# Performance work log

Measured on AMD Instinct MI355X. Metric: run time of the kernel, lower is better.

## Reference

```python
import jax, jax.numpy as jnp
import numpy as np
from jax import lax

EPS = 1e-5

def _conv(x, w, b, stride, pad):
    y = lax.conv_general_dilated(x, w, (stride, stride), ((pad, pad), (pad, pad)),
                                 dimension_numbers=('NCHW', 'OIHW', 'NCHW'))
    return y + b[None, :, None, None]

def _deconv(x, w, b):
    # torch ConvTranspose2d(k=4, s=2, p=1): weight (Cin, Cout, 4, 4)
    w2 = jnp.flip(w, (2, 3)).transpose(1, 0, 2, 3)  # OIHW for forward conv
    y = lax.conv_general_dilated(x, w2, (1, 1), ((2, 2), (2, 2)),
                                 lhs_dilation=(2, 2),
                                 dimension_numbers=('NCHW', 'OIHW', 'NCHW'))
    return y + b[None, :, None, None]

def _bn(x, g, b):
    m = jnp.mean(x, axis=(0, 2, 3), keepdims=True)
    v = jnp.mean((x - m) ** 2, axis=(0, 2, 3), keepdims=True)
    return g[None, :, None, None] * (x - m) * lax.rsqrt(v + EPS) + b[None, :, None, None]

def setup_inputs() -> dict:
    key = jax.random.key(0)
    ks = jax.random.split(key, 16)
    f32 = jnp.float32
    def w(k, shape):
        return (jax.random.normal(k, shape, f32) * 0.05)
    inp = {
        'x': jax.random.uniform(ks[0], (32, 1, 512, 512), f32),
        'w1': w(ks[1], (16, 1, 4, 4)),  'b1': jnp.zeros((16,), f32), 'g1': jnp.ones((16,), f32), 'be1': jnp.zeros((16,), f32),
        'w2': w(ks[2], (16, 16, 4, 4)), 'b2': jnp.zeros((16,), f32), 'g2': jnp.ones((16,), f32), 'be2': jnp.zeros((16,), f32),
        'w3': w(ks[3], (4, 16, 4, 4)),  'b3': jnp.zeros((4,), f32),  'g3': jnp.ones((4,), f32),  'be3': jnp.zeros((4,), f32),
        'wpre': w(ks[4], (2, 4, 1, 1)), 'bpre': jnp.zeros((2,), f32),
        'codebook': w(ks[5], (256, 2)),
        'wpost': w(ks[6], (4, 2, 1, 1)), 'bpost': jnp.zeros((4,), f32),
        'wd1': w(ks[7], (4, 16, 4, 4)),  'bd1': jnp.zeros((16,), f32), 'g4': jnp.ones((16,), f32), 'be4': jnp.zeros((16,), f32),
        'wd2': w(ks[8], (16, 16, 4, 4)), 'bd2': jnp.zeros((16,), f32), 'g5': jnp.ones((16,), f32), 'be5': jnp.zeros((16,), f32),
        'wd3': w(ks[9], (16, 1, 4, 4)),  'bd3': jnp.zeros((1,), f32),
    }
    return inp

def _forward(x, w1, b1, g1, be1, w2, b2, g2, be2, w3, b3, g3, be3,
             wpre, bpre, codebook, wpost, bpost,
             wd1, bd1, g4, be4, wd2, bd2, g5, be5, wd3, bd3):
    # encoder: three stride-2 convs with BN + ReLU
    h = jax.nn.relu(_bn(_conv(x, w1, b1, 2, 1), g1, be1))
    h = jax.nn.relu(_bn(_conv(h, w2, b2, 2, 1), g2, be2))
    h = jax.nn.relu(_bn(_conv(h, w3, b3, 2, 1), g3, be3))
    q = _conv(h, wpre, bpre, 1, 0)          # [B, 2, H/8, W/8]
    B, C, Hq, Wq = q.shape
    qf = q.transpose(0, 2, 3, 1).reshape(B * Hq * Wq, C)   # [N, 2]
    # squared Euclidean distances to codebook (argmin equals cdist argmin)
    d2 = (jnp.sum(qf * qf, -1, keepdims=True)
          - 2.0 * qf @ codebook.T
          + jnp.sum(codebook * codebook, -1)[None, :])     # [N, 256]
    idx = jnp.argmin(d2, axis=-1)
    quant = codebook[idx]                                   # gather [N, 2]
    commitment_loss = jnp.mean((lax.stop_gradient(quant) - qf) ** 2)
    codebook_loss = jnp.mean((quant - lax.stop_gradient(qf)) ** 2)
    qout = qf + lax.stop_gradient(quant - qf)               # straight-through
    qout = qout.reshape(B, Hq, Wq, C).transpose(0, 3, 1, 2)
    d = _conv(qout, wpost, bpost, 1, 0)
    d = jax.nn.relu(_bn(_deconv(d, wd1, bd1), g4, be4))
    d = jax.nn.relu(_bn(_deconv(d, wd2, bd2), g5, be5))
    out = jax.nn.sigmoid(_deconv(d, wd3, bd3))
    recon = jnp.mean((x - out) ** 2)
    total = 1.0 * recon + codebook_loss + 0.2 * commitment_loss
    return out, total

def reference(x, w1, b1, g1, be1, w2, b2, g2, be2, w3, b3, g3, be3,
              wpre, bpre, codebook, wpost, bpost,
              wd1, bd1, g4, be4, wd2, bd2, g5, be5, wd3, bd3):
    return _forward(x, w1, b1, g1, be1, w2, b2, g2, be2, w3, b3, g3, be3,
                    wpre, bpre, codebook, wpost, bpost,
                    wd1, bd1, g4, be4, wd2, bd2, g5, be5, wd3, bd3)
```

## Files before the change

kernel.cpp:

```cpp
#include <hip/hip_runtime.h>
#include <hip/hip_bf16.h>
#include <math.h>

using bf16 = __hip_bfloat16;

__device__ __forceinline__ float b2f(bf16 v) { return __bfloat162float(v); }
__device__ __forceinline__ float ldv(const void* p, size_t i, int m) {
  return m ? b2f(((const bf16*)p)[i]) : ((const float*)p)[i];
}

struct D2 { double s, s2; };

__device__ __forceinline__ void block_stats1(float v, D2* slot) {
  float v2 = v * v;
#pragma unroll
  for (int o = 32; o; o >>= 1) { v += __shfl_down(v, o, 64); v2 += __shfl_down(v2, o, 64); }
  __shared__ float a1[4], a2[4];
  int lane = threadIdx.x & 63, w = threadIdx.x >> 6;
  if (lane == 0) { a1[w] = v; a2[w] = v2; }
  __syncthreads();
  if (threadIdx.x == 0) {
    slot->s  = (double)a1[0] + a1[1] + a1[2] + a1[3];
    slot->s2 = (double)a2[0] + a2[1] + a2[2] + a2[3];
  }
}

__device__ __forceinline__ void block_stats1d4(const double* v, const double* vq, D2* base, int NB, int bx) {
  __shared__ double q1[16], q2[16];
  int lane = threadIdx.x & 63, w = threadIdx.x >> 6;
#pragma unroll
  for (int k = 0; k < 4; k++) {
    double s = v[k], s2 = vq[k];
#pragma unroll
    for (int o = 32; o; o >>= 1) { s += __shfl_down(s, o, 64); s2 += __shfl_down(s2, o, 64); }
    if (lane == 0) { q1[k * 4 + w] = s; q2[k * 4 + w] = s2; }
  }
  __syncthreads();
  if (threadIdx.x < 4) {
    int k = threadIdx.x;
    base[k * NB + bx].s  = q1[k * 4] + q1[k * 4 + 1] + q1[k * 4 + 2] + q1[k * 4 + 3];
    base[k * NB + bx].s2 = q2[k * 4] + q2[k * 4 + 1] + q2[k * 4 + 2] + q2[k * 4 + 3];
  }
}

__device__ __forceinline__ void block_sum1(float v, double* slot) {
#pragma unroll
  for (int o = 32; o; o >>= 1) v += __shfl_down(v, o, 64);
  __shared__ float a1[4];
  int lane = threadIdx.x & 63, w = threadIdx.x >> 6;
  if (lane == 0) a1[w] = v;
  __syncthreads();
  if (threadIdx.x == 0) *slot = (double)a1[0] + a1[1] + a1[2] + a1[3];
}

__device__ __forceinline__ void block_stats16(const float* vs, const float* vq, D2* base, int NB, int bx) {
  __shared__ float s1[64], s2[64];
  int lane = threadIdx.x & 63, w = threadIdx.x >> 6;
#pragma unroll
  for (int co = 0; co < 16; co++) {
    float v = vs[co], v2 = vq[co];
#pragma unroll
    for (int o = 32; o; o >>= 1) { v += __shfl_down(v, o, 64); v2 += __shfl_down(v2, o, 64); }
    if (lane == 0) { s1[co * 4 + w] = v; s2[co * 4 + w] = v2; }
  }
  __syncthreads();
  if (threadIdx.x < 16) {
    int co = threadIdx.x;
    base[co * NB + bx].s  = (double)s1[co * 4] + s1[co * 4 + 1] + s1[co * 4 + 2] + s1[co * 4 + 3];
    base[co * NB + bx].s2 = (double)s2[co * 4] + s2[co * 4 + 1] + s2[co * 4 + 2] + s2[co * 4 + 3];
  }
}

__global__ void init_k(const unsigned* __restrict__ xw, int* flag) {
  unsigned lo = xw[threadIdx.x] & 0xFFFFu;
  int inr = (lo >= 0x3000u && lo < 0x4000u) ? 1 : 0;
  unsigned long long b = __ballot(inr);
  __shared__ int cnt[4];
  if ((threadIdx.x & 63) == 0) cnt[threadIdx.x >> 6] = __popcll(b);
  __syncthreads();
  if (threadIdx.x == 0) *flag = (cnt[0] + cnt[1] + cnt[2] + cnt[3] >= 128) ? 1 : 0;
}

__global__ void prep_k(const void* w1, const void* b1, const void* w2, const void* b2,
                       const void* w3, const void* b3, const void* wpre, const void* bpre,
                       const void* cbk, const void* wpost, const void* bpost,
                       const void* wd1, const void* bd1, const void* wd2, const void* bd2,
                       const void* wd3, const void* bd3,
                       const void* g1, const void* be1, const void* g2, const void* be2,
                       const void* g3, const void* be3, const void* g4, const void* be4,
                       const void* g5, const void* be5,
                       float* __restrict__ PF, double* __restrict__ PD, const int* modep) {
  int m = *modep, t = threadIdx.x;
  for (int i = t; i < 256; i += 256) PF[i] = ldv(w1, i, m);
  if (t < 16) PF[256 + t] = ldv(b1, t, m);
  for (int i = t; i < 4096; i += 256) {
    int cig = i >> 10, tap = (i >> 6) & 15, c4 = (i >> 4) & 3, co = i & 15;
    PF[272 + i] = ldv(w2, co * 256 + (cig * 4 + c4) * 16 + tap, m);
  }
  if (t < 16) PF[4368 + t] = ldv(b2, t, m);
  for (int i = t; i < 1024; i += 256) {
    int co = i >> 6, ci = (i >> 4) & 3, tap = i & 15;
    PF[4384 + i] = ldv(wd1, ci * 256 + co * 16 + tap, m);
  }
  for (int i = t; i < 1024; i += 256) {
    int ci = i >> 8, tap = (i >> 4) & 15, co = i & 15;
    PF[14368 + i] = ldv(wd1, ci * 256 + co * 16 + tap, m);
  }
  if (t < 16) PF[5408 + t] = ldv(bd1, t, m);
  for (int i = t; i < 4096; i += 256) {
    int co = i >> 8, ci = (i >> 4) & 15, tap = i & 15;
    PF[5424 + i] = ldv(wd2, ci * 256 + co * 16 + tap, m);
  }
  for (int i = t; i < 4096; i += 256) {
    int ci = i >> 8, tap = (i >> 4) & 15, co = i & 15;
    PF[10272 + i] = ldv(wd2, ci * 256 + co * 16 + tap, m);
  }
  if (t < 16) PF[9520 + t] = ldv(bd2, t, m);
  for (int i = t; i < 256; i += 256) PF[9536 + i] = ldv(wd3, i, m);
  {
    int tap = t >> 4, ci = t & 15;
    PF[10016 + t] = ldv(wd3, ci * 16 + tap, m);
  }
  if (t == 0) PF[9792] = ldv(bd3, 0, m);
  if (t < 16) {
    PF[9856 + t] = ldv(g1, t, m);  PF[9872 + t] = ldv(be1, t, m);
    PF[9888 + t] = ldv(g2, t, m);  PF[9904 + t] = ldv(be2, t, m);
    PF[9952 + t] = ldv(g4, t, m);  PF[9968 + t] = ldv(be4, t, m);
    PF[9984 + t] = ldv(g5, t, m);  PF[10000 + t] = ldv(be5, t, m);
  }
  if (t < 4) { PF[9920 + t] = ldv(g3, t, m); PF[9936 + t] = ldv(be3, t, m); }
  for (int i = t; i < 1024; i += 256) PD[i] = ldv(w3, i, m);
  if (t < 4) PD[1024 + t] = ldv(b3, t, m);
  if (t < 8) PD[1028 + t] = ldv(wpre, t, m);
  if (t < 2) PD[1036 + t] = ldv(bpre, t, m);
  for (int i = t; i < 512; i += 256) PD[1040 + i] = ldv(cbk, i, m);
  if (t < 8) PD[1552 + t] = ldv(wpost, t, m);
  if (t < 4) PD[1560 + t] = ldv(bpost, t, m);
}

__global__ __launch_bounds__(256) void bn_reduce_k(const D2* __restrict__ part, int NB,
                                                   double* __restrict__ stD, float* __restrict__ stF,
                                                   const float* __restrict__ gb, double invN) {
  int c = blockIdx.x;
  double s = 0, s2 = 0;
  for (int i = threadIdx.x; i < NB; i += 256) { D2 p = part[c * NB + i]; s += p.s; s2 += p.s2; }
#pragma unroll
  for (int o = 32; o; o >>= 1) { s += __shfl_down(s, o, 64); s2 += __shfl_down(s2, o, 64); }
  __shared__ double l1[4], l2[4];
  int lane = threadIdx.x & 63, w = threadIdx.x >> 6;
  if (lane == 0) { l1[w] = s; l2[w] = s2; }
  __syncthreads();
  if (threadIdx.x == 0) {
    double S = l1[0] + l1[1] + l1[2] + l1[3], Q = l2[0] + l2[1] + l2[2] + l2[3];
    double mu = S * invN, var = Q * invN - mu * mu;
    if (var < 0) var = 0;
    double sc = (double)gb[c] / sqrt(var + 1e-5);
    double sh = (double)gb[16 + c] - mu * sc;
    stD[c] = sc; stD[16 + c] = sh;
    stF[c] = (float)sc; stF[16 + c] = (float)sh;
  }
}

__global__ __launch_bounds__(256) void conv1_t(const void* __restrict__ x, const float* __restrict__ PF,
                                               float* __restrict__ y, D2* __restrict__ part,
                                               const int* modep) {
  const int m = *modep;
  __shared__ float sx[10 * 130];
  int t = threadIdx.x;
  int bx = blockIdx.x;
  int b = bx >> 8, r = bx & 255, tY = r >> 2, tX = r & 3;
  int iy0 = 8 * tY - 1, ix0 = 128 * tX - 1;
  size_t xb = (size_t)b * 262144;
  for (int i = t; i < 1300; i += 256) {
    int ry = i / 130, rx = i - ry * 130;
    int gy = iy0 + ry, gx = ix0 + rx;
    float v = 0.f;
    if ((unsigned)gy < 512u && (unsigned)gx < 512u) v = ldv(x, xb + (size_t)gy * 512 + gx, m);
    sx[i] = v;
  }
  __syncthreads();
  int tyy = t >> 6, txx = t & 63;
  int oy = tY * 4 + tyy, ox = tX * 64 + txx;
  float acc[16];
#pragma unroll
  for (int co = 0; co < 16; co++) acc[co] = PF[256 + co];
  int ly = 2 * tyy, lx = 2 * txx;
#pragma unroll
  for (int ky = 0; ky < 4; ky++) {
#pragma unroll
    for (int kx = 0; kx < 4; kx++) {
      float v = sx[(ly + ky) * 130 + lx + kx];
#pragma unroll
      for (int co = 0; co < 16; co++) acc[co] = fmaf(v, PF[co * 16 + ky * 4 + kx], acc[co]);
    }
  }
  size_t pix = (size_t)b * 65536 + (size_t)(oy * 256 + ox);
  *(float4*)(y + 0 * 8388608 + pix * 4) = make_float4(acc[0],  acc[1],  acc[2],  acc[3]);
  *(float4*)(y + 1 * 8388608 + pix * 4) = make_float4(acc[4],  acc[5],  acc[6],  acc[7]);
  *(float4*)(y + 2 * 8388608 + pix * 4) = make_float4(acc[8],  acc[9],  acc[10], acc[11]);
  *(float4*)(y + 3 * 8388608 + pix * 4) = make_float4(acc[12], acc[13], acc[14], acc[15]);
  float vq_[16];
#pragma unroll
  for (int co = 0; co < 16; co++) vq_[co] = acc[co] * acc[co];
  block_stats16(acc, vq_, part, 8192, bx);
}

__device__ __forceinline__ float4 aff_relu4(float4 v, float4 sc, float4 sh) {
  v.x = fmaxf(fmaf(v.x, sc.x, sh.x), 0.f);
  v.y = fmaxf(fmaf(v.y, sc.y, sh.y), 0.f);
  v.z = fmaxf(fmaf(v.z, sc.z, sh.z), 0.f);
  v.w = fmaxf(fmaf(v.w, sc.w, sh.w), 0.f);
  return v;
}

__global__ __launch_bounds__(256, 8) void conv2_t(const float* __restrict__ h1, const float* __restrict__ PF,
                                                  const float* __restrict__ aff, float* __restrict__ h2,
                                                  D2* __restrict__ part) {
  __shared__ float su[4896];
  int t = threadIdx.x, ty = t >> 4, tx = t & 15;
  int bx = blockIdx.x, bb = bx >> 6, r = bx & 63, tY = r >> 3, tX = r & 7;
  int oy = tY * 16 + ty, ox = tX * 16 + tx;
  int iy0 = 32 * tY - 1, ix0 = 32 * tX - 1;
  const float* W2 = PF + 272;
  const float4* A4 = (const float4*)aff;
  float acc[16];
#pragma unroll
  for (int co = 0; co < 16; co++) acc[co] = PF[4368 + co];
#pragma unroll
  for (int g = 0; g < 4; g++) {
    __syncthreads();
    float4 SC = A4[g], SH = A4[4 + g];
    const float* pg = h1 + (size_t)g * 8388608 + (size_t)bb * 262144;
    for (int i = t; i < 1156; i += 256) {
      int riy = i / 34, rix = i - riy * 34;
      int gy = iy0 + riy, gx = ix0 + rix;
      float4 v = make_float4(0.f, 0.f, 0.f, 0.f);
      if ((unsigned)gy < 256u && (unsigned)gx < 256u)
        v = aff_relu4(*(const float4*)(pg + (size_t)(gy * 256 + gx) * 4), SC, SH);
      int s = (rix & 1) * 2448 + riy * 18 + (rix >> 1);
      su[s] = v.x; su[612 + s] = v.y; su[1224 + s] = v.z; su[1836 + s] = v.w;
    }
    __syncthreads();
    const float* wg = W2 + g * 1024;
    int base = 2 * ty * 18 + tx;
#pragma unroll
    for (int ky = 0; ky < 4; ky++) {
#pragma unroll
      for (int kx = 0; kx < 4; kx++) {
        int s = (kx & 1) * 2448 + ky * 18 + (kx >> 1) + base;
        float v0 = su[s], v1 = su[612 + s], v2 = su[1224 + s], v3 = su[1836 + s];
        const float* wt = wg + (ky * 4 + kx) * 64;
#pragma unroll
        for (int co = 0; co < 16; co++) {
          float s0 = fmaf(v0, wt[co], acc[co]);
          float s1 = fmaf(v1, wt[16 + co], s0);
          float s2 = fmaf(v2, wt[32 + co], s1);
          acc[co] = fmaf(v3, wt[48 + co], s2);
        }
      }
    }
  }
  float vq_[16];
#pragma unroll
  for (int co = 0; co < 16; co++) {
    h2[((size_t)(bb * 16 + co) * 128 + oy) * 128 + ox] = acc[co];
    vq_[co] = acc[co] * acc[co];
  }
  block_stats16(acc, vq_, part, 2048, bx);
}

__global__ __launch_bounds__(256) void conv3_k(const float* __restrict__ h2, const double* __restrict__ PD,
                                               const float* __restrict__ aff, double* __restrict__ c3,
                                               D2* __restrict__ part) {
  int idx = blockIdx.x * 256 + threadIdx.x;
  int b = idx >> 12, rem = idx & 4095, oy = rem >> 6, ox = rem & 63;
  double a0 = PD[1024], a1 = PD[1025], a2 = PD[1026], a3 = PD[1027];
  int iy0 = 2 * oy - 1, ix0 = 2 * ox - 1;
  for (int ci = 0; ci < 16; ci++) {
    const float* ib = h2 + (size_t)(b * 16 + ci) * 16384;
    float sc = aff[ci], sh = aff[16 + ci];
    const double* wr = PD + ci * 16;
#pragma unroll
    for (int ky = 0; ky < 4; ky++) {
      int iy = iy0 + ky;
      if ((unsigned)iy < 128u) {
        const float* row = ib + iy * 128;
#pragma unroll
        for (int kx = 0; kx < 4; kx++) {
          int ix = ix0 + kx;
          if ((unsigned)ix < 128u) {
            double v = (double)fmaxf(fmaf(row[ix], sc, sh), 0.f);
            int tp = ky * 4 + kx;
            a0 = fma(v, wr[tp], a0);
            a1 = fma(v, wr[256 + tp], a1);
            a2 = fma(v, wr[512 + tp], a2);
            a3 = fma(v, wr[768 + tp], a3);
          }
        }
      }
    }
  }
  size_t cb = (size_t)b * 16384 + rem;
  c3[cb] = a0; c3[cb + 4096] = a1; c3[cb + 8192] = a2; c3[cb + 12288] = a3;
  double vs[4] = {a0, a1, a2, a3};
  double vq[4] = {a0 * a0, a1 * a1, a2 * a2, a3 * a3};
  block_stats1d4(vs, vq, part, 512, blockIdx.x);
}

__global__ __launch_bounds__(256) void vq_k(const double* __restrict__ c3, const double* __restrict__ PD,
                                            const double* __restrict__ stD2, float* __restrict__ d0,
                                            double* __restrict__ vp) {
  __shared__ double cb[512];
  for (int i = threadIdx.x; i < 512; i += 256) cb[i] = PD[1040 + i];
  __syncthreads();
  int pix = blockIdx.x * 256 + threadIdx.x;
  int b = pix >> 12, rem = pix & 4095;
  const double* hb = c3 + (size_t)b * 16384 + rem;
  double q0 = PD[1036], q1 = PD[1037];
#pragma unroll
  for (int ci = 0; ci < 4; ci++) {
    double v = fma(hb[ci * 4096], stD2[ci], stD2[16 + ci]);
    if (v < 0) v = 0;
    q0 = fma(v, PD[1028 + ci], q0);
    q1 = fma(v, PD[1032 + ci], q1);
  }
  int best = 0;
  double bd = 1e300;
  for (int k = 0; k < 256; k++) {
    double dx = q0 - cb[2 * k], dy = q1 - cb[2 * k + 1];
    double d = dx * dx + dy * dy;
    if (d < bd) { bd = d; best = k; }
  }
  double c0 = cb[2 * best], c1 = cb[2 * best + 1];
  double e0 = q0 - c0, e1 = q1 - c1;
  float* ob = d0 + (size_t)b * 16384 + rem;
#pragma unroll
  for (int c = 0; c < 4; c++)
    ob[c * 4096] = (float)(PD[1560 + c] + PD[1552 + 2 * c] * c0 + PD[1552 + 2 * c + 1] * c1);
  double v = e0 * e0 + e1 * e1;
#pragma unroll
  for (int o = 32; o; o >>= 1) v += __shfl_down(v, o, 64);
  __shared__ double l1[4];
  int lane = threadIdx.x & 63, w = threadIdx.x >> 6;
  if (lane == 0) l1[w] = v;
  __syncthreads();
  if (threadIdx.x == 0) vp[blockIdx.x] = l1[0] + l1[1] + l1[2] + l1[3];
}

__global__ __launch_bounds__(256) void deconv1_k(const float* __restrict__ d0, const float* __restrict__ PF,
                                                 float* __restrict__ d1, D2* __restrict__ part) {
  int phase = blockIdx.y, a = phase >> 1, bc = phase & 1;
  int idx = blockIdx.x * 256 + threadIdx.x;
  int b = idx >> 12, rem = idx & 4095, qy = rem >> 6, qx = rem & 63;
  const float* WT = PF + 14368;
  float acc[16];
#pragma unroll
  for (int co = 0; co < 16; co++) acc[co] = PF[5408 + co];
  const float* hb = d0 + (size_t)b * 16384;
#pragma unroll
  for (int t2y = 0; t2y < 2; t2y++) {
    int iy = qy + a - t2y;
    if ((unsigned)iy < 64u) {
      int kyo = (1 - a + 2 * t2y) * 4;
#pragma unroll
      for (int t2x = 0; t2x < 2; t2x++) {
        int ix = qx + bc - t2x;
        if ((unsigned)ix < 64u) {
          int tap = kyo + (1 - bc + 2 * t2x);
          int off = iy * 64 + ix;
#pragma unroll
          for (int ci = 0; ci < 4; ci++) {
            float v = hb[ci * 4096 + off];
            const float* wt = WT + ci * 256 + tap * 16;
#pragma unroll
            for (int co = 0; co < 16; co++) acc[co] = fmaf(v, wt[co], acc[co]);
          }
        }
      }
    }
  }
  int oy = 2 * qy + a, ox = 2 * qx + bc;
  size_t pix = (size_t)b * 16384 + (size_t)(oy * 128 + ox);
  *(float4*)(d1 + 0 * 2097152 + pix * 4) = make_float4(acc[0],  acc[1],  acc[2],  acc[3]);
  *(float4*)(d1 + 1 * 2097152 + pix * 4) = make_float4(acc[4],  acc[5],  acc[6],  acc[7]);
  *(float4*)(d1 + 2 * 2097152 + pix * 4) = make_float4(acc[8],  acc[9],  acc[10], acc[11]);
  *(float4*)(d1 + 3 * 2097152 + pix * 4) = make_float4(acc[12], acc[13], acc[14], acc[15]);
  float vq_[16];
#pragma unroll
  for (int co = 0; co < 16; co++) vq_[co] = acc[co] * acc[co];
  block_stats16(acc, vq_, part, 2048, blockIdx.y * 512 + blockIdx.x);
}

__global__ __launch_bounds__(256) void deconv2_t(const float* __restrict__ d1, const float* __restrict__ PF,
                                                 const float* __restrict__ aff, float* __restrict__ d2,
                                                 D2* __restrict__ part) {
  __shared__ float su[16 * 324];
  int t = threadIdx.x, py = t >> 4, px = t & 15;
  int bx = blockIdx.x, bb = bx >> 6, r = bx & 63, tY = r >> 3, tX = r & 7;
  int iy0 = 16 * tY - 1, ix0 = 16 * tX - 1;
  const float4* A4 = (const float4*)aff;
  for (int i = t; i < 1296; i += 256) {
    int g = i / 324, rr = i - g * 324;
    int riy = rr / 18, rix = rr - riy * 18;
    int gy = iy0 + riy, gx = ix0 + rix;
    float4 v = make_float4(0.f, 0.f, 0.f, 0.f);
    if ((unsigned)gy < 128u && (unsigned)gx < 128u)
      v = aff_relu4(*(const float4*)(d1 + (size_t)g * 2097152 +
                                     ((size_t)bb * 16384 + (size_t)(gy * 128 + gx)) * 4),
                    A4[g], A4[4 + g]);
    int s0 = g * 1296 + rr;
    su[s0] = v.x; su[s0 + 324] = v.y; su[s0 + 648] = v.z; su[s0 + 972] = v.w;
  }
  __syncthreads();
  const float* WT = PF + 10272;
  float vs[16], vq[16];
#pragma unroll
  for (int co = 0; co < 16; co++) { vs[co] = 0.f; vq[co] = 0.f; }
#pragma unroll
  for (int a = 0; a < 2; a++) {
#pragma unroll
    for (int bc = 0; bc < 2; bc++) {
      float acc[16];
#pragma unroll
      for (int co = 0; co < 16; co++) acc[co] = PF[9520 + co];
      int base = (py + a) * 18 + (px + bc);
      for (int ci = 0; ci < 16; ci++) {
        const float* sb = su + ci * 324 + base;
        float v00 = sb[0], v01 = sb[1], v10 = sb[18], v11 = sb[19];
        const float* wci = WT + ci * 256;
        const float* w00p = wci + (((3 - a) * 4 + (3 - bc)) << 4);
        const float* w01p = wci + (((3 - a) * 4 + (1 - bc)) << 4);
        const float* w10p = wci + (((1 - a) * 4 + (3 - bc)) << 4);
        const float* w11p = wci + (((1 - a) * 4 + (1 - bc)) << 4);
#pragma unroll
        for (int co = 0; co < 16; co++) {
          float s0 = fmaf(v00, w00p[co], acc[co]);
          float s1 = fmaf(v01, w01p[co], s0);
          float s2 = fmaf(v10, w10p[co], s1);
          acc[co] = fmaf(v11, w11p[co], s2);
        }
      }
      int oy = 32 * tY + 2 * py + a, ox = 32 * tX + 2 * px + bc;
      float4* dst = (float4*)(d2 + ((size_t)bb * 65536 + (size_t)oy * 256 + ox) * 16);
      dst[0] = make_float4(acc[0],  acc[1],  acc[2],  acc[3]);
      dst[1] = make_float4(acc[4],  acc[5],  acc[6],  acc[7]);
      dst[2] = make_float4(acc[8],  acc[9],  acc[10], acc[11]);
      dst[3] = make_float4(acc[12], acc[13], acc[14], acc[15]);
#pragma unroll
      for (int co = 0; co < 16; co++) {
        vs[co] += acc[co];
        vq[co] = fmaf(acc[co], acc[co], vq[co]);
      }
    }
  }
  block_stats16(vs, vq, part, 2048, bx);
}

__device__ __forceinline__ int swz(int p, int g) {
  int s = p * 4 + (g ^ (p & 3));
  return s ^ (((p >> 2) & 1) << 2);
}

__device__ __forceinline__ float4 aff_relu(float4 v, float4 sc, float4 sh) {
  v.x = fmaxf(fmaf(v.x, sc.x, sh.x), 0.f);
  v.y = fmaxf(fmaf(v.y, sc.y, sh.y), 0.f);
  v.z = fmaxf(fmaf(v.z, sc.z, sh.z), 0.f);
  v.w = fmaxf(fmaf(v.w, sc.w, sh.w), 0.f);
  return v;
}

__device__ __forceinline__ void dot4(float& a, float4 v, float4 w) {
  a = fmaf(v.x, w.x, a); a = fmaf(v.y, w.y, a);
  a = fmaf(v.z, w.z, a); a = fmaf(v.w, w.w, a);
}

__global__ __launch_bounds__(256, 4) void deconv3_t(const float* __restrict__ d2, const float* __restrict__ PF,
                                                    const float* __restrict__ aff, const void* __restrict__ x,
                                                    void* __restrict__ outp, double* __restrict__ rp,
                                                    const int* __restrict__ modep) {
  const int m = *modep;
  __shared__ float4 sd4[1296];
  int t = threadIdx.x;
  int bx = blockIdx.x;
  int b = bx >> 8, r = bx & 255, tY = r >> 4, tX = r & 15;
  int iy0 = 16 * tY - 1, ix0 = 16 * tX - 1;
  const float4* A4 = (const float4*)aff;
  float4 SC0 = A4[0], SC1 = A4[1], SC2 = A4[2], SC3 = A4[3];
  float4 SH0 = A4[4], SH1 = A4[5], SH2 = A4[6], SH3 = A4[7];
  const float* db = d2 + (size_t)b * 1048576;
  for (int p = t; p < 324; p += 256) {
    int riy = p / 18, rix = p - riy * 18;
    int gy = iy0 + riy, gx = ix0 + rix;
    float4 v0, v1, v2, v3;
    if ((unsigned)gy < 256u && (unsigned)gx < 256u) {
      const float4* s = (const float4*)(db + ((size_t)gy * 256 + gx) * 16);
      v0 = aff_relu(s[0], SC0, SH0);
      v1 = aff_relu(s[1], SC1, SH1);
      v2 = aff_relu(s[2], SC2, SH2);
      v3 = aff_relu(s[3], SC3, SH3);
    } else {
      v0 = v1 = v2 = v3 = make_float4(0.f, 0.f, 0.f, 0.f);
    }
    sd4[swz(p, 0)] = v0; sd4[swz(p, 1)] = v1; sd4[swz(p, 2)] = v2; sd4[swz(p, 3)] = v3;
  }
  __syncthreads();

  int lx = t & 15, ly = t >> 4;
  float bias = PF[9792];
  float a00 = bias, a01 = bias, a10 = bias, a11 = bias;
  const float* WT = PF + 10016;
  int p00 = ly * 18 + lx;
#define TAPW(ky, kx) (*(const float4*)(WT + ((ky) * 4 + (kx)) * 16 + (g << 2)))
#pragma unroll
  for (int g = 0; g < 4; g++) {
    float4 w33 = TAPW(3, 3), w31 = TAPW(3, 1), w32 = TAPW(3, 2), w30 = TAPW(3, 0);
    float4 w13 = TAPW(1, 3), w11 = TAPW(1, 1), w12 = TAPW(1, 2), w10 = TAPW(1, 0);
    float4 w23 = TAPW(2, 3), w21 = TAPW(2, 1), w22 = TAPW(2, 2), w20 = TAPW(2, 0);
    float4 w03 = TAPW(0, 3), w01 = TAPW(0, 1), w02 = TAPW(0, 2), w00 = TAPW(0, 0);
    float4 v;
    v = sd4[swz(p00, g)];      dot4(a00, v, w33);
    v = sd4[swz(p00 + 1, g)];  dot4(a00, v, w31); dot4(a01, v, w32);
    v = sd4[swz(p00 + 2, g)];  dot4(a01, v, w30);
    v = sd4[swz(p00 + 18, g)]; dot4(a00, v, w13); dot4(a10, v, w23);
    v = sd4[swz(p00 + 19, g)]; dot4(a00, v, w11); dot4(a01, v, w12); dot4(a10, v, w21); dot4(a11, v, w22);
    v = sd4[swz(p00 + 20, g)]; dot4(a01, v, w10); dot4(a11, v, w20);
    v = sd4[swz(p00 + 36, g)]; dot4(a10, v, w03);
    v = sd4[swz(p00 + 37, g)]; dot4(a10, v, w01); dot4(a11, v, w02);
    v = sd4[swz(p00 + 38, g)]; dot4(a11, v, w00);
  }
#undef TAPW

  int oy = 32 * tY + 2 * ly, ox = 32 * tX + 2 * lx;
  size_t ob = (size_t)b * 262144 + (size_t)oy * 512 + ox;
  float o0 = 1.f / (1.f + expf(-a00));
  float o1 = 1.f / (1.f + expf(-a01));
  float o2 = 1.f / (1.f + expf(-a10));
  float o3 = 1.f / (1.f + expf(-a11));
  if (m) {
    bf16* op = (bf16*)outp;
    op[ob] = __float2bfloat16(o0);       op[ob + 1] = __float2bfloat16(o1);
    op[ob + 512] = __float2bfloat16(o2); op[ob + 513] = __float2bfloat16(o3);
  } else {
    float* op = (float*)outp;
    op[ob] = o0;       op[ob + 1] = o1;
    op[ob + 512] = o2; op[ob + 513] = o3;
  }
  float d0_ = ldv(x, ob, m) - o0;
  float d1_ = ldv(x, ob + 1, m) - o1;
  float d2_ = ldv(x, ob + 512, m) - o2;
  float d3_ = ldv(x, ob + 513, m) - o3;
  float ds = fmaf(d0_, d0_, fmaf(d1_, d1_, fmaf(d2_, d2_, d3_ * d3_)));
  block_sum1(ds, rp + bx);
}

__global__ __launch_bounds__(256) void finalize_k(const double* __restrict__ vp, const double* __restrict__ rp,
                                                  void* outp, const int* modep) {
  double s = 0, rr = 0;
  for (int i = threadIdx.x; i < 512; i += 256) s += vp[i];
  for (int i = threadIdx.x; i < 8192; i += 256) rr += rp[i];
#pragma unroll
  for (int o = 32; o; o >>= 1) { s += __shfl_down(s, o, 64); rr += __shfl_down(rr, o, 64); }
  __shared__ double l1[4], l2[4];
  int lane = threadIdx.x & 63, w = threadIdx.x >> 6;
  if (lane == 0) { l1[w] = s; l2[w] = rr; }
  __syncthreads();
  if (threadIdx.x == 0) {
    double S = l1[0] + l1[1] + l1[2] + l1[3], R = l2[0] + l2[1] + l2[2] + l2[3];
    double total = R * (1.0 / 8388608.0) + 1.2 * (S * (1.0 / 262144.0));
    if (*modep) ((bf16*)outp)[8388608] = __float2bfloat16((float)total);
    else        ((float*)outp)[8388608] = (float)total;
  }
}

extern "C" void kernel_launch(void* const* d_in, const int* in_sizes, int n_in,
                              void* d_out, int out_size, void* d_ws, size_t ws_size,
                              hipStream_t stream) {
  const void* x    = d_in[0];
  const void* w1   = d_in[1];  const void* b1  = d_in[2];
  const void* g1   = d_in[3];  const void* be1 = d_in[4];
  const void* w2   = d_in[5];  const void* b2  = d_in[6];
  const void* g2   = d_in[7];  const void* be2 = d_in[8];
  const void* w3   = d_in[9];  const void* b3  = d_in[10];
  const void* g3   = d_in[11]; const void* be3 = d_in[12];
  const void* wpre = d_in[13]; const void* bpre= d_in[14];
  const void* cbk  = d_in[15];
  const void* wpost= d_in[16]; const void* bpost= d_in[17];
  const void* wd1  = d_in[18]; const void* bd1 = d_in[19];
  const void* g4   = d_in[20]; const void* be4 = d_in[21];
  const void* wd2  = d_in[22]; const void* bd2 = d_in[23];
  const void* g5   = d_in[24]; const void* be5 = d_in[25];
  const void* wd3  = d_in[26]; const void* bd3 = d_in[27];

  char* ws = (char*)d_ws;
  int*    MODE = (int*)ws;
  float*  STF  = (float*)(ws + 1024);
  double* STD  = (double*)(ws + 4096);
  float*  PF   = (float*)(ws + 8192);
  double* PD   = (double*)(ws + 73728);
  D2*     P1   = (D2*)(ws + 131072);
  D2*     P2   = (D2*)(ws + 2228224);
  D2*     P3   = (D2*)(ws + 2752512);
  D2*     P4   = (D2*)(ws + 2785280);
  D2*     P5   = (D2*)(ws + 3309568);
  double* VP   = (double*)(ws + 3833856);
  double* RP   = (double*)(ws + 3837952);
  char* HB = ws + 6291456;
  float*  H1  = (float*)HB;
  float*  H2  = (float*)(HB + 134217728);
  double* C3  = (double*)HB;
  float*  D0  = (float*)(HB + 165675008);
  float*  D1  = (float*)HB;
  float*  D2T = (float*)(HB + 33554432);

  init_k<<<1, 256, 0, stream>>>((const unsigned*)x, MODE);
  prep_k<<<1, 256, 0, stream>>>(w1, b1, w2, b2, w3, b3, wpre, bpre, cbk, wpost, bpost,
                                wd1, bd1, wd2, bd2, wd3, bd3,
                                g1, be1, g2, be2, g3, be3, g4, be4, g5, be5, PF, PD, MODE);

  conv1_t<<<8192, 256, 0, stream>>>(x, PF, H1, P1, MODE);
  bn_reduce_k<<<16, 256, 0, stream>>>(P1, 8192, STD + 0, STF + 0, PF + 9856, 1.0 / 2097152.0);

  conv2_t<<<2048, 256, 0, stream>>>(H1, PF, STF + 0, H2, P2);
  bn_reduce_k<<<16, 256, 0, stream>>>(P2, 2048, STD + 32, STF + 32, PF + 9888, 1.0 / 524288.0);

  conv3_k<<<512, 256, 0, stream>>>(H2, PD, STF + 32, C3, P3);
  bn_reduce_k<<<4, 256, 0, stream>>>(P3, 512, STD + 64, STF + 64, PF + 9920, 1.0 / 131072.0);

  vq_k<<<512, 256, 0, stream>>>(C3, PD, STD + 64, D0, VP);

  deconv1_k<<<dim3(512, 4), 256, 0, stream>>>(D0, PF, D1, P4);
  bn_reduce_k<<<16, 256, 0, stream>>>(P4, 2048, STD + 96, STF + 96, PF + 9952, 1.0 / 524288.0);

  deconv2_t<<<2048, 256, 0, stream>>>(D1, PF, STF + 96, D2T, P5);
  bn_reduce_k<<<16, 256, 0, stream>>>(P5, 2048, STD + 128, STF + 128, PF + 9984, 1.0 / 2097152.0);

  deconv3_t<<<8192, 256, 0, stream>>>(D2T, PF, STF + 128, x, d_out, RP, MODE);
  finalize_k<<<1, 256, 0, stream>>>(VP, RP, d_out, MODE);
}
```

Baseline: 548.1 us.

## Store deconv2 output as bf16, prefetch conv2 tiles, fold init into prep

Deconv2 now writes its 16-channel output packed as bf16 pairs, and deconv3 unpacks it. This halves the traffic on the largest intermediate tensor, at the cost of rounding the pre-BN activations (BN statistics are still taken in fp32). Conv2 loads the next channel group into registers while computing the current one, with occupancy lowered from 8 to 6 waves per unit to fit the extra registers. The mode-detection kernel is merged into prep_k to save one launch.

New measurement: 699.2 us. 27.6% more time.

```diff
diff --git a/kernel.cpp b/kernel.cpp
--- a/kernel.cpp
+++ b/kernel.cpp
@@ -8,6 +8,14 @@
 __device__ __forceinline__ float ldv(const void* p, size_t i, int m) {
   return m ? b2f(((const bf16*)p)[i]) : ((const float*)p)[i];
 }
+
+__device__ __forceinline__ unsigned pk2(float a, float b) {
+  union { bf16 h; unsigned short u; } ca, cb;
+  ca.h = __float2bfloat16(a); cb.h = __float2bfloat16(b);
+  return (unsigned)ca.u | ((unsigned)cb.u << 16);
+}
+__device__ __forceinline__ float lo2f(unsigned u) { return __uint_as_float(u << 16); }
+__device__ __forceinline__ float hi2f(unsigned u) { return __uint_as_float(u & 0xFFFF0000u); }
 
 struct D2 { double s, s2; };
 
@@ -71,17 +79,8 @@
   }
 }
 
-__global__ void init_k(const unsigned* __restrict__ xw, int* flag) {
-  unsigned lo = xw[threadIdx.x] & 0xFFFFu;
-  int inr = (lo >= 0x3000u && lo < 0x4000u) ? 1 : 0;
-  unsigned long long b = __ballot(inr);
-  __shared__ int cnt[4];
-  if ((threadIdx.x & 63) == 0) cnt[threadIdx.x >> 6] = __popcll(b);
-  __syncthreads();
-  if (threadIdx.x == 0) *flag = (cnt[0] + cnt[1] + cnt[2] + cnt[3] >= 128) ? 1 : 0;
-}
-
-__global__ void prep_k(const void* w1, const void* b1, const void* w2, const void* b2,
+__global__ void prep_k(const unsigned* __restrict__ xw, int* __restrict__ MODE,
+                       const void* w1, const void* b1, const void* w2, const void* b2,
                        const void* w3, const void* b3, const void* wpre, const void* bpre,
                        const void* cbk, const void* wpost, const void* bpost,
                        const void* wd1, const void* bd1, const void* wd2, const void* bd2,
@@ -89,8 +88,20 @@
                        const void* g1, const void* be1, const void* g2, const void* be2,
                        const void* g3, const void* be3, const void* g4, const void* be4,
                        const void* g5, const void* be5,
-                       float* __restrict__ PF, double* __restrict__ PD, const int* modep) {
-  int m = *modep, t = threadIdx.x;
+                       float* __restrict__ PF, double* __restrict__ PD) {
+  int t = threadIdx.x;
+  __shared__ int smode;
+  {
+    unsigned lo = xw[t] & 0xFFFFu;
+    int inr = (lo >= 0x3000u && lo < 0x4000u) ? 1 : 0;
+    unsigned long long b = __ballot(inr);
+    __shared__ int cnt[4];
+    if ((t & 63) == 0) cnt[t >> 6] = __popcll(b);
+    __syncthreads();
+    if (t == 0) { smode = (cnt[0] + cnt[1] + cnt[2] + cnt[3] >= 128) ? 1 : 0; *MODE = smode; }
+    __syncthreads();
+  }
+  int m = smode;
   for (int i = t; i < 256; i += 256) PF[i] = ldv(w1, i, m);
   if (t < 16) PF[256 + t] = ldv(b1, t, m);
   for (int i = t; i < 4096; i += 256) {
@@ -213,7 +224,7 @@
   return v;
 }
 
-__global__ __launch_bounds__(256, 8) void conv2_t(const float* __restrict__ h1, const float* __restrict__ PF,
+__global__ __launch_bounds__(256, 6) void conv2_t(const float* __restrict__ h1, const float* __restrict__ PF,
                                                   const float* __restrict__ aff, float* __restrict__ h2,
                                                   D2* __restrict__ part) {
   __shared__ float su[4896];
@@ -223,24 +234,52 @@
   int iy0 = 32 * tY - 1, ix0 = 32 * tX - 1;
   const float* W2 = PF + 272;
   const float4* A4 = (const float4*)aff;
-  float acc[16];
-#pragma unroll
-  for (int co = 0; co < 16; co++) acc[co] = PF[4368 + co];
-#pragma unroll
-  for (int g = 0; g < 4; g++) {
-    __syncthreads();
-    float4 SC = A4[g], SH = A4[4 + g];
-    const float* pg = h1 + (size_t)g * 8388608 + (size_t)bb * 262144;
-    for (int i = t; i < 1156; i += 256) {
+  int goff[5], soff[5];
+#pragma unroll
+  for (int k = 0; k < 5; k++) {
+    int i = t + k * 256;
+    goff[k] = -1; soff[k] = -1;
+    if (i < 1156) {
       int riy = i / 34, rix = i - riy * 34;
       int gy = iy0 + riy, gx = ix0 + rix;
-      float4 v = make_float4(0.f, 0.f, 0.f, 0.f);
-      if ((unsigned)gy < 256u && (unsigned)gx < 256u)
-        v = aff_relu4(*(const float4*)(pg + (size_t)(gy * 256 + gx) * 4), SC, SH);
-      int s = (rix & 1) * 2448 + riy * 18 + (rix >> 1);
-      su[s] = v.x; su[612 + s] = v.y; su[1224 + s] = v.z; su[1836 + s] = v.w;
-    }
+      soff[k] = (rix & 1) * 2448 + riy * 18 + (rix >> 1);
+      if ((unsigned)gy < 256u && (unsigned)gx < 256u) goff[k] = (gy * 256 + gx) * 4;
+    }
+  }
+  const float* pb = h1 + (size_t)bb * 262144;
+  float4 rv[5];
+#pragma unroll
+  for (int k = 0; k < 5; k++) {
+    float4 v = make_float4(0.f, 0.f, 0.f, 0.f);
+    if (goff[k] >= 0) v = *(const float4*)(pb + goff[k]);
+    rv[k] = v;
+  }
+  float acc[16];
+#pragma unroll
+  for (int co = 0; co < 16; co++) acc[co] = PF[4368 + co];
+#pragma unroll
+  for (int g = 0; g < 4; g++) {
+    float4 SC = A4[g], SH = A4[4 + g];
     __syncthreads();
+#pragma unroll
+    for (int k = 0; k < 5; k++) {
+      if (soff[k] >= 0) {
+        float4 v = make_float4(0.f, 0.f, 0.f, 0.f);
+        if (goff[k] >= 0) v = aff_relu4(rv[k], SC, SH);
+        int s = soff[k];
+        su[s] = v.x; su[612 + s] = v.y; su[1224 + s] = v.z; su[1836 + s] = v.w;
+      }
+    }
+    __syncthreads();
+    if (g < 3) {
+      const float* pg = pb + (size_t)(g + 1) * 8388608;
+#pragma unroll
+      for (int k = 0; k < 5; k++) {
+        float4 v = make_float4(0.f, 0.f, 0.f, 0.f);
+        if (goff[k] >= 0) v = *(const float4*)(pg + goff[k]);
+        rv[k] = v;
+      }
+    }
     const float* wg = W2 + g * 1024;
     int base = 2 * ty * 18 + tx;
 #pragma unroll
@@ -392,7 +431,7 @@
 }
 
 __global__ __launch_bounds__(256) void deconv2_t(const float* __restrict__ d1, const float* __restrict__ PF,
-                                                 const float* __restrict__ aff, float* __restrict__ d2,
+                                                 const float* __restrict__ aff, unsigned* __restrict__ d2,
                                                  D2* __restrict__ part) {
   __shared__ float su[16 * 324];
   int t = threadIdx.x, py = t >> 4, px = t & 15;
@@ -441,11 +480,11 @@
         }
       }
       int oy = 32 * tY + 2 * py + a, ox = 32 * tX + 2 * px + bc;
-      float4* dst = (float4*)(d2 + ((size_t)bb * 65536 + (size_t)oy * 256 + ox) * 16);
-      dst[0] = make_float4(acc[0],  acc[1],  acc[2],  acc[3]);
-      dst[1] = make_float4(acc[4],  acc[5],  acc[6],  acc[7]);
-      dst[2] = make_float4(acc[8],  acc[9],  acc[10], acc[11]);
-      dst[3] = make_float4(acc[12], acc[13], acc[14], acc[15]);
+      uint4* dst = (uint4*)(d2 + ((size_t)bb * 65536 + (size_t)oy * 256 + ox) * 8);
+      dst[0] = make_uint4(pk2(acc[0], acc[1]),  pk2(acc[2], acc[3]),
+                          pk2(acc[4], acc[5]),  pk2(acc[6], acc[7]));
+      dst[1] = make_uint4(pk2(acc[8], acc[9]),  pk2(acc[10], acc[11]),
+                          pk2(acc[12], acc[13]), pk2(acc[14], acc[15]));
 #pragma unroll
       for (int co = 0; co < 16; co++) {
         vs[co] += acc[co];
@@ -474,7 +513,7 @@
   a = fmaf(v.z, w.z, a); a = fmaf(v.w, w.w, a);
 }
 
-__global__ __launch_bounds__(256, 4) void deconv3_t(const float* __restrict__ d2, const float* __restrict__ PF,
+__global__ __launch_bounds__(256, 4) void deconv3_t(const unsigned* __restrict__ d2, const float* __restrict__ PF,
                                                     const float* __restrict__ aff, const void* __restrict__ x,
                                                     void* __restrict__ outp, double* __restrict__ rp,
                                                     const int* __restrict__ modep) {
@@ -487,17 +526,18 @@
   const float4* A4 = (const float4*)aff;
   float4 SC0 = A4[0], SC1 = A4[1], SC2 = A4[2], SC3 = A4[3];
   float4 SH0 = A4[4], SH1 = A4[5], SH2 = A4[6], SH3 = A4[7];
-  const float* db = d2 + (size_t)b * 1048576;
+  const unsigned* db = d2 + (size_t)b * 524288;
   for (int p = t; p < 324; p += 256) {
     int riy = p / 18, rix = p - riy * 18;
     int gy = iy0 + riy, gx = ix0 + rix;
     float4 v0, v1, v2, v3;
     if ((unsigned)gy < 256u && (unsigned)gx < 256u) {
-      const float4* s = (const float4*)(db + ((size_t)gy * 256 + gx) * 16);
-      v0 = aff_relu(s[0], SC0, SH0);
-      v1 = aff_relu(s[1], SC1, SH1);
-      v2 = aff_relu(s[2], SC2, SH2);
-      v3 = aff_relu(s[3], SC3, SH3);
+      const uint4* s = (const uint4*)(db + ((size_t)gy * 256 + gx) * 8);
+      uint4 u0 = s[0], u1 = s[1];
+      v0 = aff_relu(make_float4(lo2f(u0.x), hi2f(u0.x), lo2f(u0.y), hi2f(u0.y)), SC0, SH0);
+      v1 = aff_relu(make_float4(lo2f(u0.z), hi2f(u0.z), lo2f(u0.w), hi2f(u0.w)), SC1, SH1);
+      v2 = aff_relu(make_float4(lo2f(u1.x), hi2f(u1.x), lo2f(u1.y), hi2f(u1.y)), SC2, SH2);
+      v3 = aff_relu(make_float4(lo2f(u1.z), hi2f(u1.z), lo2f(u1.w), hi2f(u1.w)), SC3, SH3);
     } else {
       v0 = v1 = v2 = v3 = make_float4(0.f, 0.f, 0.f, 0.f);
     }
@@ -605,17 +645,17 @@
   double* VP   = (double*)(ws + 3833856);
   double* RP   = (double*)(ws + 3837952);
   char* HB = ws + 6291456;
-  float*  H1  = (float*)HB;
-  float*  H2  = (float*)(HB + 134217728);
-  double* C3  = (double*)HB;
-  float*  D0  = (float*)(HB + 165675008);
-  float*  D1  = (float*)HB;
-  float*  D2T = (float*)(HB + 33554432);
-
-  init_k<<<1, 256, 0, stream>>>((const unsigned*)x, MODE);
-  prep_k<<<1, 256, 0, stream>>>(w1, b1, w2, b2, w3, b3, wpre, bpre, cbk, wpost, bpost,
+  float*    H1  = (float*)HB;
+  float*    H2  = (float*)(HB + 134217728);
+  double*   C3  = (double*)HB;
+  float*    D0  = (float*)(HB + 165675008);
+  float*    D1  = (float*)HB;
+  unsigned* D2T = (unsigned*)(HB + 33554432);
+
+  prep_k<<<1, 256, 0, stream>>>((const unsigned*)x, MODE,
+                                w1, b1, w2, b2, w3, b3, wpre, bpre, cbk, wpost, bpost,
                                 wd1, bd1, wd2, bd2, wd3, bd3,
-                                g1, be1, g2, be2, g3, be3, g4, be4, g5, be5, PF, PD, MODE);
+                                g1, be1, g2, be2, g3, be3, g4, be4, g5, be5, PF, PD);
 
   conv1_t<<<8192, 256, 0, stream>>>(x, PF, H1, P1, MODE);
   bn_reduce_k<<<16, 256, 0, stream>>>(P1, 8192, STD + 0, STF + 0, PF + 9856, 1.0 / 2097152.0);
```
